# Kernel tuning notes

Hardware: AMD Instinct MI355X
Metric: run time of the kernel (lower is better)

The kernel has to match this reference:

```python
import jax, jax.numpy as jnp
import numpy as np

N_NODES = 50000
N_EDGES = 800000
IN_DIM, HID_DIM, OUT_DIM = 128, 96, 96
NUM_GRAPHS = 64
NEG_SLOPE_ATT = 0.2   # GATConv internal leaky_relu
NEG_SLOPE_ACT = 0.01  # F.leaky_relu default between layers


def setup_inputs() -> dict:
    key = jax.random.key(0)
    ks = jax.random.split(key, 16)
    x = jax.random.normal(ks[0], (N_NODES, IN_DIM), dtype=jnp.float32)
    edge_index = jax.random.randint(ks[1], (2, N_EDGES), 0, N_NODES, dtype=jnp.int64)
    batch = jnp.sort(jax.random.randint(ks[2], (N_NODES,), 0, NUM_GRAPHS, dtype=jnp.int64))

    def glorot(k, shape):
        lim = np.sqrt(6.0 / (shape[0] + shape[-1]))
        return jax.random.uniform(k, shape, jnp.float32, -lim, lim)

    params = {}
    dims = [(IN_DIM, HID_DIM), (HID_DIM, HID_DIM), (HID_DIM, OUT_DIM)]
    for i, (di, do) in enumerate(dims, start=1):
        params[f"W{i}"] = glorot(ks[3 * i], (di, do))
        params[f"a_src{i}"] = glorot(ks[3 * i + 1], (do,))
        params[f"a_dst{i}"] = glorot(ks[3 * i + 2], (do,))
        params[f"b{i}"] = jnp.zeros((do,), jnp.float32)
    return {"x": x, "edge_index": edge_index, "batch": batch, **params}


def gat_conv(x, src, dst, W, a_src, a_dst, b):
    # x: [N, in], src/dst: [Etot] (self-loops included)
    h = x @ W                                   # [N, out]
    alpha_s = h @ a_src                         # [N]
    alpha_d = h @ a_dst                         # [N]
    e = jax.nn.leaky_relu(alpha_s[src] + alpha_d[dst], NEG_SLOPE_ATT)  # [Etot]
    # segment softmax over destination neighborhoods
    m = jax.ops.segment_max(e, dst, num_segments=N_NODES)
    ex = jnp.exp(e - m[dst])
    denom = jax.ops.segment_sum(ex, dst, num_segments=N_NODES)
    alpha = ex / (denom[dst] + 1e-16)           # [Etot]
    msg = alpha[:, None] * h[src]               # [Etot, out]
    out = jax.ops.segment_sum(msg, dst, num_segments=N_NODES)
    return out + b


def reference(x, edge_index, batch, W1, a_src1, a_dst1, b1, W2, a_src2, a_dst2, b2, W3, a_src3, a_dst3, b3):
    # add self loops once (PyG GATConv add_self_loops=True per layer; same edge set)
    sl = jnp.arange(N_NODES, dtype=edge_index.dtype)
    src = jnp.concatenate([edge_index[0], sl])
    dst = jnp.concatenate([edge_index[1], sl])

    h = jax.nn.leaky_relu(gat_conv(x, src, dst, W1, a_src1, a_dst1, b1), NEG_SLOPE_ACT)
    h = jax.nn.leaky_relu(gat_conv(h, src, dst, W2, a_src2, a_dst2, b2), NEG_SLOPE_ACT)
    h = gat_conv(h, src, dst, W3, a_src3, a_dst3, b3)

    # global mean pool over graphs
    sums = jax.ops.segment_sum(h, batch, num_segments=NUM_GRAPHS)       # [G, out]
    counts = jax.ops.segment_sum(jnp.ones((N_NODES,), h.dtype), batch, num_segments=NUM_GRAPHS)
    return sums / jnp.maximum(counts, 1.0)[:, None]
```

## Files before the change

### kernel.cpp

```cpp
#include <hip/hip_runtime.h>

#define N_NODES 50000
#define N_EDGES 800000
#define E_TOT   850000
#define IN0     128
#define HID     96
#define NUM_GRAPHS 64
#define NB      ((N_NODES + 1023) / 1024)

__device__ __forceinline__ float leaky(float x, float s) { return x > 0.f ? x : s * x; }

__global__ void count_deg(const int* __restrict__ dst, int* __restrict__ deg) {
    int e = blockIdx.x * blockDim.x + threadIdx.x;
    if (e >= E_TOT) return;
    int d = (e < N_EDGES) ? dst[e] : (e - N_EDGES);
    atomicAdd(&deg[d], 1);
}

__global__ __launch_bounds__(256) void block_sums(const int* __restrict__ deg, int* __restrict__ bsum) {
    int b = blockIdx.x, t = threadIdx.x;
    int base = b * 1024 + t * 4;
    int s = 0;
    if (base + 3 < N_NODES) {
        int4 v = *(const int4*)(deg + base);
        s = v.x + v.y + v.z + v.w;
    } else {
        for (int k = 0; k < 4; ++k) if (base + k < N_NODES) s += deg[base + k];
    }
#pragma unroll
    for (int w = 32; w >= 1; w >>= 1) s += __shfl_xor(s, w);
    __shared__ int ws[4];
    if ((t & 63) == 0) ws[t >> 6] = s;
    __syncthreads();
    if (t == 0) bsum[b] = ws[0] + ws[1] + ws[2] + ws[3];
}

__global__ void scan_partials(const int* __restrict__ bsum, int* __restrict__ excl, int* __restrict__ offs) {
    int t = threadIdx.x;
    int v = (t < NB) ? bsum[t] : 0;
    int incl = v;
#pragma unroll
    for (int d = 1; d < 64; d <<= 1) {
        int u = __shfl_up(incl, d);
        if (t >= d) incl += u;
    }
    if (t < NB) excl[t] = incl - v;
    if (t == 0) offs[N_NODES] = E_TOT;
}

__global__ __launch_bounds__(256) void write_offs(const int* __restrict__ deg,
                                                  const int* __restrict__ excl,
                                                  int* __restrict__ offs) {
    __shared__ int sh[256];
    int b = blockIdx.x, t = threadIdx.x;
    int base = b * 1024 + t * 4;
    int d0 = 0, d1 = 0, d2 = 0, d3 = 0;
    if (base + 3 < N_NODES) {
        int4 v = *(const int4*)(deg + base);
        d0 = v.x; d1 = v.y; d2 = v.z; d3 = v.w;
    } else {
        if (base     < N_NODES) d0 = deg[base];
        if (base + 1 < N_NODES) d1 = deg[base + 1];
        if (base + 2 < N_NODES) d2 = deg[base + 2];
    }
    int tsum = d0 + d1 + d2 + d3;
    sh[t] = tsum;
    __syncthreads();
    for (int off = 1; off < 256; off <<= 1) {
        int u = (t >= off) ? sh[t - off] : 0;
        __syncthreads();
        sh[t] += u;
        __syncthreads();
    }
    int ebase = excl[b] + sh[t] - tsum;
    if (base + 3 < N_NODES) {
        int4 o; o.x = ebase; o.y = ebase + d0; o.z = ebase + d0 + d1; o.w = ebase + d0 + d1 + d2;
        *(int4*)(offs + base) = o;
    } else {
        if (base     < N_NODES) offs[base]     = ebase;
        if (base + 1 < N_NODES) offs[base + 1] = ebase + d0;
        if (base + 2 < N_NODES) offs[base + 2] = ebase + d0 + d1;
    }
}

__global__ void scatter_edges(const int* __restrict__ src, const int* __restrict__ dst,
                              const int* __restrict__ offs, int* __restrict__ cursor,
                              int* __restrict__ csr) {
    int e = blockIdx.x * blockDim.x + threadIdx.x;
    if (e >= E_TOT) return;
    int s, d;
    if (e < N_EDGES) { s = src[e]; d = dst[e]; }
    else             { s = e - N_EDGES; d = s; }
    int pos = offs[d] + atomicAdd(&cursor[d], 1);
    csr[pos] = s;
}

template <int IN>
__global__ __launch_bounds__(256) void gemm_alpha(
    const float* __restrict__ X, const float* __restrict__ W,
    const float* __restrict__ asrc, const float* __restrict__ adst,
    float* __restrict__ H, float* __restrict__ As, float* __restrict__ Ad) {
    __shared__ float Ws[IN * HID];
    __shared__ float Xs[32 * IN];
    int t = threadIdx.x;
    int rowBase = blockIdx.x * 32;
    for (int idx = t; idx < IN * HID; idx += 256) Ws[idx] = W[idx];
    for (int idx = t; idx < 32 * IN; idx += 256) {
        int r = idx / IN, c = idx - r * IN;
        int gr = rowBase + r;
        Xs[idx] = (gr < N_NODES) ? X[gr * IN + c] : 0.f;
    }
    __syncthreads();
    int r = t >> 5;
    int lane = t & 31;
    int c = lane * 3;
    float acc[4][3];
#pragma unroll
    for (int i = 0; i < 4; ++i)
#pragma unroll
        for (int j = 0; j < 3; ++j) acc[i][j] = 0.f;
#pragma unroll 4
    for (int k = 0; k < IN; ++k) {
        float w0 = Ws[k * HID + c], w1 = Ws[k * HID + c + 1], w2 = Ws[k * HID + c + 2];
#pragma unroll
        for (int i = 0; i < 4; ++i) {
            float xv = Xs[(r + 8 * i) * IN + k];
            acc[i][0] += xv * w0; acc[i][1] += xv * w1; acc[i][2] += xv * w2;
        }
    }
    float a0 = asrc[c], a1 = asrc[c + 1], a2 = asrc[c + 2];
    float d0 = adst[c], d1 = adst[c + 1], d2 = adst[c + 2];
#pragma unroll
    for (int i = 0; i < 4; ++i) {
        int row = rowBase + r + 8 * i;
        if (row < N_NODES) {
            H[row * HID + c]     = acc[i][0];
            H[row * HID + c + 1] = acc[i][1];
            H[row * HID + c + 2] = acc[i][2];
            float ps = acc[i][0] * a0 + acc[i][1] * a1 + acc[i][2] * a2;
            float pd = acc[i][0] * d0 + acc[i][1] * d1 + acc[i][2] * d2;
#pragma unroll
            for (int m = 16; m >= 1; m >>= 1) {
                ps += __shfl_xor(ps, m);
                pd += __shfl_xor(pd, m);
            }
            if (lane == 0) { As[row] = ps; Ad[row] = pd; }
        }
    }
}

__global__ __launch_bounds__(256) void aggregate(
    const float* __restrict__ H, const float* __restrict__ As, const float* __restrict__ Ad,
    const int* __restrict__ offs, const int* __restrict__ csr,
    const float* __restrict__ bias, float* __restrict__ Hout, int apply_leaky) {
    int team = (blockIdx.x * blockDim.x + threadIdx.x) >> 5;
    int lane = threadIdx.x & 31;
    int half = threadIdx.x & 32;
    int start = offs[team], end = offs[team + 1];
    float ad = Ad[team];
    float m = leaky(As[team] + ad, 0.2f);
    float acc0 = 0.f, acc1 = 0.f, acc2 = 0.f, denom = 0.f;
    int c = lane * 3;
    for (int base = start; base < end; base += 32) {
        int i = base + lane;
        bool valid = i < end;
        int s = valid ? csr[i] : 0;
        float ex = 0.f;
        if (valid) ex = __expf(leaky(As[s] + ad, 0.2f) - m);
        denom += ex;
        int cnt = min(32, end - base);
        int j = 0;
        for (; j + 8 <= cnt; j += 8) {
            float e[8]; int ss[8];
#pragma unroll
            for (int q = 0; q < 8; ++q) {
                e[q]  = __shfl(ex, half + j + q);
                ss[q] = __shfl(s,  half + j + q);
            }
            float v0[8], v1[8], v2[8];
#pragma unroll
            for (int q = 0; q < 8; ++q) {
                const float* p = H + (size_t)ss[q] * HID + c;
                v0[q] = p[0]; v1[q] = p[1]; v2[q] = p[2];
            }
#pragma unroll
            for (int q = 0; q < 8; ++q) {
                acc0 += e[q] * v0[q]; acc1 += e[q] * v1[q]; acc2 += e[q] * v2[q];
            }
        }
        for (; j + 4 <= cnt; j += 4) {
            float e[4]; int ss[4];
#pragma unroll
            for (int q = 0; q < 4; ++q) {
                e[q]  = __shfl(ex, half + j + q);
                ss[q] = __shfl(s,  half + j + q);
            }
            float v0[4], v1[4], v2[4];
#pragma unroll
            for (int q = 0; q < 4; ++q) {
                const float* p = H + (size_t)ss[q] * HID + c;
                v0[q] = p[0]; v1[q] = p[1]; v2[q] = p[2];
            }
#pragma unroll
            for (int q = 0; q < 4; ++q) {
                acc0 += e[q] * v0[q]; acc1 += e[q] * v1[q]; acc2 += e[q] * v2[q];
            }
        }
        for (; j < cnt; ++j) {
            float bex = __shfl(ex, half + j);
            int   bs  = __shfl(s,  half + j);
            const float* hp = H + (size_t)bs * HID + c;
            acc0 += bex * hp[0]; acc1 += bex * hp[1]; acc2 += bex * hp[2];
        }
    }
#pragma unroll
    for (int w = 16; w >= 1; w >>= 1) denom += __shfl_xor(denom, w);
    float inv = 1.f / (denom + 1e-16f);
    float o0 = acc0 * inv + bias[c];
    float o1 = acc1 * inv + bias[c + 1];
    float o2 = acc2 * inv + bias[c + 2];
    if (apply_leaky) { o0 = leaky(o0, 0.01f); o1 = leaky(o1, 0.01f); o2 = leaky(o2, 0.01f); }
    Hout[team * HID + c]     = o0;
    Hout[team * HID + c + 1] = o1;
    Hout[team * HID + c + 2] = o2;
}

__global__ __launch_bounds__(256) void pool_sum(
    const float* __restrict__ H, const int* __restrict__ batch,
    float* __restrict__ sums, float* __restrict__ counts) {
    int team = (blockIdx.x * blockDim.x + threadIdx.x) >> 5;
    int lane = threadIdx.x & 31;
    int c = lane * 3;
    int n0 = team * 32;
    if (n0 >= N_NODES) return;
    int n1 = min(n0 + 32, N_NODES);
    float a0 = 0.f, a1 = 0.f, a2 = 0.f;
    int cur = batch[n0], runlen = 0;
    for (int n = n0; n < n1; ++n) {
        int g = batch[n];
        if (g != cur) {
            atomicAdd(&sums[cur * HID + c],     a0);
            atomicAdd(&sums[cur * HID + c + 1], a1);
            atomicAdd(&sums[cur * HID + c + 2], a2);
            if (lane == 0) atomicAdd(&counts[cur], (float)runlen);
            a0 = a1 = a2 = 0.f; cur = g; runlen = 0;
        }
        const float* hp = H + (size_t)n * HID + c;
        a0 += hp[0]; a1 += hp[1]; a2 += hp[2];
        ++runlen;
    }
    atomicAdd(&sums[cur * HID + c],     a0);
    atomicAdd(&sums[cur * HID + c + 1], a1);
    atomicAdd(&sums[cur * HID + c + 2], a2);
    if (lane == 0) atomicAdd(&counts[cur], (float)runlen);
}

__global__ void finalize(const float* __restrict__ sums, const float* __restrict__ counts,
                         float* __restrict__ out) {
    int i = blockIdx.x * blockDim.x + threadIdx.x;
    if (i < NUM_GRAPHS * HID) out[i] = sums[i] / fmaxf(counts[i / HID], 1.f);
}

extern "C" void kernel_launch(void* const* d_in, const int* in_sizes, int n_in,
                              void* d_out, int out_size, void* d_ws, size_t ws_size,
                              hipStream_t stream) {
    const float* x     = (const float*)d_in[0];
    const int*   ei    = (const int*)d_in[1];
    const int*   srcI  = ei;
    const int*   dstI  = ei + N_EDGES;
    const int*   batch = (const int*)d_in[2];
    const float* W1 = (const float*)d_in[3],  *as1 = (const float*)d_in[4],
               * ad1 = (const float*)d_in[5], *b1  = (const float*)d_in[6];
    const float* W2 = (const float*)d_in[7],  *as2 = (const float*)d_in[8],
               * ad2 = (const float*)d_in[9], *b2  = (const float*)d_in[10];
    const float* W3 = (const float*)d_in[11], *as3 = (const float*)d_in[12],
               * ad3 = (const float*)d_in[13], *b3 = (const float*)d_in[14];
    float* out = (float*)d_out;

    char* p = (char*)d_ws;
    float* h0 = (float*)p;  p += (size_t)N_NODES * HID * 4;
    float* h1 = (float*)p;  p += (size_t)N_NODES * HID * 4;
    float* As = (float*)p;  p += (size_t)N_NODES * 4;
    float* Ad = (float*)p;  p += (size_t)N_NODES * 4;
    int* offs = (int*)p;    p += (size_t)(N_NODES + 4) * 4;
    int* csr  = (int*)p;    p += (size_t)E_TOT * 4;
    int* bsum = (int*)p;    p += 64 * 4;
    int* excl = (int*)p;    p += 64 * 4;
    char* zbase = p;
    float* sums   = (float*)p; p += (size_t)NUM_GRAPHS * HID * 4;
    float* counts = (float*)p; p += (size_t)NUM_GRAPHS * 4;
    int* deg    = (int*)p;  p += (size_t)N_NODES * 4;
    int* cursor = (int*)p;  p += (size_t)N_NODES * 4;
    size_t zbytes = (size_t)(p - zbase);

    hipMemsetAsync(zbase, 0, zbytes, stream);

    int eb = (E_TOT + 255) / 256;
    count_deg<<<eb, 256, 0, stream>>>(dstI, deg);
    block_sums<<<NB, 256, 0, stream>>>(deg, bsum);
    scan_partials<<<1, 64, 0, stream>>>(bsum, excl, offs);
    write_offs<<<NB, 256, 0, stream>>>(deg, excl, offs);
    scatter_edges<<<eb, 256, 0, stream>>>(srcI, dstI, offs, cursor, csr);

    int gemmGrid = (N_NODES + 31) / 32;
    int aggGrid  = (N_NODES * 32) / 256;

    gemm_alpha<IN0><<<gemmGrid, 256, 0, stream>>>(x, W1, as1, ad1, h0, As, Ad);
    aggregate<<<aggGrid, 256, 0, stream>>>(h0, As, Ad, offs, csr, b1, h1, 1);
    gemm_alpha<HID><<<gemmGrid, 256, 0, stream>>>(h1, W2, as2, ad2, h0, As, Ad);
    aggregate<<<aggGrid, 256, 0, stream>>>(h0, As, Ad, offs, csr, b2, h1, 1);
    gemm_alpha<HID><<<gemmGrid, 256, 0, stream>>>(h1, W3, as3, ad3, h0, As, Ad);
    aggregate<<<aggGrid, 256, 0, stream>>>(h0, As, Ad, offs, csr, b3, h1, 0);

    int teams = (N_NODES + 31) / 32;
    pool_sum<<<(teams * 32 + 255) / 256, 256, 0, stream>>>(h1, batch, sums, counts);
    finalize<<<(NUM_GRAPHS * HID + 255) / 256, 256, 0, stream>>>(sums, counts, out);
}
```

Before: 455.0 us.

## Replace shared-memory tiled GEMM with per-thread row-wise register GEMM

Rewrites the feature-transform kernel so that each thread computes 24 output columns of one row. X is read straight from global memory as float4 and W is read through the cache instead of being staged into LDS, and the attention dot products are reduced across the four column groups through a small shared buffer. This drops the large LDS footprint (up to 80KB per block before) and the serial staging step, which should raise occupancy. In exchange, W is reloaded from global/L1 per thread, the uncoalesced per-row X loads may stress the cache, and the 24-float accumulator adds register pressure.

```diff
diff --git a/kernel.cpp b/kernel.cpp
--- a/kernel.cpp
+++ b/kernel.cpp
@@ -96,55 +96,54 @@
 }
 
 template <int IN>
-__global__ __launch_bounds__(256) void gemm_alpha(
+__global__ __launch_bounds__(256) void gemm_rowwise(
     const float* __restrict__ X, const float* __restrict__ W,
     const float* __restrict__ asrc, const float* __restrict__ adst,
     float* __restrict__ H, float* __restrict__ As, float* __restrict__ Ad) {
-    __shared__ float Ws[IN * HID];
-    __shared__ float Xs[32 * IN];
+    __shared__ float asP[256], adP[256];
     int t = threadIdx.x;
-    int rowBase = blockIdx.x * 32;
-    for (int idx = t; idx < IN * HID; idx += 256) Ws[idx] = W[idx];
-    for (int idx = t; idx < 32 * IN; idx += 256) {
-        int r = idx / IN, c = idx - r * IN;
-        int gr = rowBase + r;
-        Xs[idx] = (gr < N_NODES) ? X[gr * IN + c] : 0.f;
-    }
+    int q = t >> 6;
+    int r = t & 63;
+    int row = blockIdx.x * 64 + r;
+    int cbase = q * 24;
+    bool valid = row < N_NODES;
+    float ps = 0.f, pd = 0.f;
+    if (valid) {
+        const float* xr = X + (size_t)row * IN;
+        const float* wq = W + cbase;
+        float acc[24];
+#pragma unroll
+        for (int c = 0; c < 24; ++c) acc[c] = 0.f;
+        for (int k = 0; k < IN; k += 4) {
+            float4 xv = *(const float4*)(xr + k);
+            const float* wp = wq + (size_t)k * HID;
+#pragma unroll
+            for (int c = 0; c < 24; ++c) {
+                acc[c] += xv.x * wp[c];
+                acc[c] += xv.y * wp[c + HID];
+                acc[c] += xv.z * wp[c + 2 * HID];
+                acc[c] += xv.w * wp[c + 3 * HID];
+            }
+        }
+        float* hr = H + (size_t)row * HID + cbase;
+#pragma unroll
+        for (int c = 0; c < 24; c += 4) {
+            float4 o; o.x = acc[c]; o.y = acc[c + 1]; o.z = acc[c + 2]; o.w = acc[c + 3];
+            *(float4*)(hr + c) = o;
+        }
+#pragma unroll
+        for (int c = 0; c < 24; ++c) {
+            ps += acc[c] * asrc[cbase + c];
+            pd += acc[c] * adst[cbase + c];
+        }
+    }
+    asP[t] = ps; adP[t] = pd;
     __syncthreads();
-    int r = t >> 5;
-    int lane = t & 31;
-    int c = lane * 3;
-    float acc[4][3];
-#pragma unroll
-    for (int i = 0; i < 4; ++i)
-#pragma unroll
-        for (int j = 0; j < 3; ++j) acc[i][j] = 0.f;
-#pragma unroll 4
-    for (int k = 0; k < IN; ++k) {
-        float w0 = Ws[k * HID + c], w1 = Ws[k * HID + c + 1], w2 = Ws[k * HID + c + 2];
-#pragma unroll
-        for (int i = 0; i < 4; ++i) {
-            float xv = Xs[(r + 8 * i) * IN + k];
-            acc[i][0] += xv * w0; acc[i][1] += xv * w1; acc[i][2] += xv * w2;
-        }
-    }
-    float a0 = asrc[c], a1 = asrc[c + 1], a2 = asrc[c + 2];
-    float d0 = adst[c], d1 = adst[c + 1], d2 = adst[c + 2];
-#pragma unroll
-    for (int i = 0; i < 4; ++i) {
-        int row = rowBase + r + 8 * i;
-        if (row < N_NODES) {
-            H[row * HID + c]     = acc[i][0];
-            H[row * HID + c + 1] = acc[i][1];
-            H[row * HID + c + 2] = acc[i][2];
-            float ps = acc[i][0] * a0 + acc[i][1] * a1 + acc[i][2] * a2;
-            float pd = acc[i][0] * d0 + acc[i][1] * d1 + acc[i][2] * d2;
-#pragma unroll
-            for (int m = 16; m >= 1; m >>= 1) {
-                ps += __shfl_xor(ps, m);
-                pd += __shfl_xor(pd, m);
-            }
-            if (lane == 0) { As[row] = ps; Ad[row] = pd; }
+    if (t < 64) {
+        int row0 = blockIdx.x * 64 + t;
+        if (row0 < N_NODES) {
+            As[row0] = asP[t] + asP[64 + t] + asP[128 + t] + asP[192 + t];
+            Ad[row0] = adP[t] + adP[64 + t] + adP[128 + t] + adP[192 + t];
         }
     }
 }
@@ -302,14 +301,14 @@
     write_offs<<<NB, 256, 0, stream>>>(deg, excl, offs);
     scatter_edges<<<eb, 256, 0, stream>>>(srcI, dstI, offs, cursor, csr);
 
-    int gemmGrid = (N_NODES + 31) / 32;
+    int gemmGrid = (N_NODES + 63) / 64;
     int aggGrid  = (N_NODES * 32) / 256;
 
-    gemm_alpha<IN0><<<gemmGrid, 256, 0, stream>>>(x, W1, as1, ad1, h0, As, Ad);
+    gemm_rowwise<IN0><<<gemmGrid, 256, 0, stream>>>(x, W1, as1, ad1, h0, As, Ad);
     aggregate<<<aggGrid, 256, 0, stream>>>(h0, As, Ad, offs, csr, b1, h1, 1);
-    gemm_alpha<HID><<<gemmGrid, 256, 0, stream>>>(h1, W2, as2, ad2, h0, As, Ad);
+    gemm_rowwise<HID><<<gemmGrid, 256, 0, stream>>>(h1, W2, as2, ad2, h0, As, Ad);
     aggregate<<<aggGrid, 256, 0, stream>>>(h0, As, Ad, offs, csr, b2, h1, 1);
-    gemm_alpha<HID><<<gemmGrid, 256, 0, stream>>>(h1, W3, as3, ad3, h0, As, Ad);
+    gemm_rowwise<HID><<<gemmGrid, 256, 0, stream>>>(h1, W3, as3, ad3, h0, As, Ad);
     aggregate<<<aggGrid, 256, 0, stream>>>(h0, As, Ad, offs, csr, b3, h1, 0);
 
     int teams = (N_NODES + 31) / 32;
```

New measurement: 606.9 us. +33.4%, slower.
